# Kernel tuning notes

Measured on AMD Instinct MI355X. Metric: run time of the kernel, lower is better.

Reference implementation:

```python
import jax, jax.numpy as jnp
import numpy as np

NB_HEAD = 16
SIZE_PER_HEAD = 64


def setup_inputs() -> dict:
    key = jax.random.key(0)
    k1, k2 = jax.random.split(key)
    x = jax.random.normal(k1, (2, 2048, 1024), dtype=jnp.float32)
    kernel = jax.random.normal(k2, (3, 1024, NB_HEAD * SIZE_PER_HEAD), dtype=jnp.float32) * 0.02
    return {"x": x, "kernel": kernel}


def reference(x, kernel):
    B, S, D = x.shape
    H, dh = NB_HEAD, SIZE_PER_HEAD
    # QKV projections: [B,S,D] @ [D, H*dh] -> [B,S,H,dh] -> [B,H,S,dh]
    def proj(w):
        return jnp.einsum('bsd,de->bse', x, w).reshape(B, S, H, dh).transpose(0, 2, 1, 3)
    Q = proj(kernel[0])
    Ks = proj(kernel[1])
    V = proj(kernel[2])
    scores = jnp.einsum('bhqd,bhkd->bhqk', Q, Ks) / jnp.sqrt(jnp.float32(dh))
    attn = jax.nn.softmax(scores, axis=-1)
    z = jnp.einsum('bhqk,bhkd->bhqd', attn, V)  # [B,H,S,dh]
    return z.transpose(0, 2, 1, 3).reshape(B, S, H * dh)
```

## Files before the change

### kernel.cpp

```cpp
#include <hip/hip_runtime.h>
#include <hip/hip_bf16.h>

#define HB 16
#define DH 64
#define SQ 2048
#define BB 2

using f32x4 = __attribute__((ext_vector_type(4))) float;
using f32x16 = __attribute__((ext_vector_type(16))) float;
using s16x8 = __attribute__((ext_vector_type(8))) short;

__device__ __forceinline__ unsigned bfr(float f) {
    union { float f; unsigned u; } v; v.f = f;
    return (v.u + 0x7fffu + ((v.u >> 16) & 1u)) >> 16;
}
__device__ __forceinline__ unsigned pk2(float a, float b) { return bfr(a) | (bfr(b) << 16); }
__device__ __forceinline__ short f2bf(float f) { return (short)bfr(f); }

__device__ __forceinline__ int swz64(int r, int c) {
    return r * 64 + ((((c >> 3) ^ (r & 7)) & 7) << 3) + (c & 7);
}
__device__ __forceinline__ int swz32(int r, int c) {
    return r * 32 + ((((c >> 3) ^ ((r >> 1) & 3)) & 3) << 3) + (c & 7);
}

__device__ __forceinline__ void gll16(const short* g, short* l) {
    __builtin_amdgcn_global_load_lds(
        (const __attribute__((address_space(1))) unsigned int*)(uintptr_t)g,
        (__attribute__((address_space(3))) unsigned int*)(uintptr_t)l, 16, 0, 0);
}

__device__ __forceinline__ int swzT(int n, int k) {
    return n * 64 + ((((k >> 3) ^ ((n >> 2) & 7)) & 7) << 3) + (k & 7);
}
__global__ __launch_bounds__(256) void cvt_all(
    const float* __restrict__ x, const float* __restrict__ w,
    short* __restrict__ xb, short* __restrict__ wt)
{
    __shared__ short T[64 * 64];
    int bid = blockIdx.x;
    int t = threadIdx.x;
    if (bid < 2048) {
        int i = (bid * 256 + t) * 8;
        float4 v0 = *(const float4*)&x[i];
        float4 v1 = *(const float4*)&x[i + 4];
        uint4 u;
        u.x = pk2(v0.x, v0.y); u.y = pk2(v0.z, v0.w);
        u.z = pk2(v1.x, v1.y); u.w = pk2(v1.z, v1.w);
        *(uint4*)&xb[i] = u;
        return;
    }
    bid -= 2048;
    int nt = bid & 15, kt = (bid >> 4) & 15, p = bid >> 8;
    const float* wp = w + p * 1048576 + (kt * 64) * 1024 + nt * 64;
    short* wtp = wt + p * 1048576 + (nt * 64) * 1024 + kt * 64;
#pragma unroll
    for (int ps = 0; ps < 4; ps++) {
        int idx = ps * 1024 + t * 4;
        int r = idx >> 6, c = idx & 63;
        float4 v = *(const float4*)&wp[r * 1024 + c];
        T[swzT(c + 0, r)] = f2bf(v.x);
        T[swzT(c + 1, r)] = f2bf(v.y);
        T[swzT(c + 2, r)] = f2bf(v.z);
        T[swzT(c + 3, r)] = f2bf(v.w);
    }
    __syncthreads();
#pragma unroll
    for (int ps = 0; ps < 2; ps++) {
        int idx = ps * 2048 + t * 8;
        int n = idx >> 6, kc = idx & 63;
        s16x8 vv = *(const s16x8*)&T[swzT(n, kc)];
        *(s16x8*)&wtp[n * 1024 + kc] = vv;
    }
}

__global__ __launch_bounds__(512, 1) void qkv_gemm(
    const short* __restrict__ xb, const short* __restrict__ wt, short* __restrict__ ws)
{
    __shared__ short Xs[3][128 * 32];
    __shared__ short Ns[3][384 * 32];
    const int tid = threadIdx.x;
    const int wv = tid >> 6, ln = tid & 63;
    const int bid = blockIdx.x;
    const int swz = (bid & 7) * 32 + (bid >> 3);
    const int m0 = (swz & 31) * 128;
    const int n0 = (swz >> 5) * 128;

    const int wm = (wv >> 2) * 64, wn = (wv & 3) * 96;
    const int lr = ln & 15, lk = (ln >> 4) * 8;
    const int srow = tid >> 2;
    const int csw = (((tid & 3) ^ ((tid >> 3) & 3)) & 3) * 8;

    f32x4 acc[4][6] = {};

#define GSTAGE(k0_, bf_) do {                                                   \
        gll16(&xb[(m0 + srow) * 1024 + (k0_) + csw], &Xs[bf_][wv * 512]);       \
        _Pragma("unroll")                                                       \
        for (int p_ = 0; p_ < 3; p_++)                                          \
            gll16(&wt[p_ * 1048576 + (n0 + srow) * 1024 + (k0_) + csw],         \
                  &Ns[bf_][p_ * 4096 + wv * 512]);                              \
    } while (0)

#define GCOMP(bf_) do {                                                         \
        s16x8 af[4], bg[6];                                                     \
        _Pragma("unroll")                                                       \
        for (int i = 0; i < 4; i++)                                             \
            af[i] = *(const s16x8*)&Xs[bf_][swz32(wm + i * 16 + lr, lk)];       \
        _Pragma("unroll")                                                       \
        for (int j = 0; j < 6; j++)                                             \
            bg[j] = *(const s16x8*)&Ns[bf_][swz32(wn + j * 16 + lr, lk)];       \
        __builtin_amdgcn_s_setprio(1);                                          \
        _Pragma("unroll")                                                       \
        for (int i = 0; i < 4; i++)                                             \
            _Pragma("unroll")                                                   \
            for (int j = 0; j < 6; j++)                                         \
                acc[i][j] = __builtin_amdgcn_mfma_f32_16x16x32_bf16(af[i], bg[j], acc[i][j], 0, 0, 0); \
        __builtin_amdgcn_s_setprio(0);                                          \
    } while (0)

    GSTAGE(0, 0);
    GSTAGE(32, 1);
    int cur = 0;
    for (int t = 0; t < 31; t++) {
        asm volatile("s_waitcnt vmcnt(4)\n\ts_barrier" ::: "memory");
        int pre = cur + 2; if (pre >= 3) pre -= 3;
        if (t < 30) GSTAGE((t + 2) * 32, pre);
        GCOMP(cur);
        cur = (cur == 2) ? 0 : cur + 1;
    }
    asm volatile("s_waitcnt vmcnt(0)\n\ts_barrier" ::: "memory");
    GCOMP(cur);

    short* qws = ws;
    short* kws = ws + BB * HB * SQ * DH;
    short* vtw = ws + 2 * BB * HB * SQ * DH;
#pragma unroll
    for (int i = 0; i < 4; i++) {
#pragma unroll
        for (int r = 0; r < 4; r++) {
            int row = m0 + wm + i * 16 + (ln >> 4) * 4 + r;
            int b = row >> 11, s = row & 2047;
#pragma unroll
            for (int j = 0; j < 6; j++) {
                int c = wn + j * 16 + (ln & 15);
                int p = c >> 7;
                int gcol = n0 + (c & 127);
                int h = gcol >> 6, dhi = gcol & 63;
                float v = acc[i][j][r];
                if (p == 0)      qws[((b * HB + h) * SQ + s) * DH + dhi] = f2bf(v * 0.1803368801f);
                else if (p == 1) kws[((b * HB + h) * SQ + s) * DH + dhi] = f2bf(v);
                else             vtw[((b * HB + h) * DH + dhi) * SQ + s] = f2bf(v);
            }
        }
    }
#undef GSTAGE
#undef GCOMP
}

__global__ __launch_bounds__(512) void attn(
    const short* __restrict__ qws, const short* __restrict__ kws,
    const short* __restrict__ vtw, float* __restrict__ out)
{
    __shared__ __align__(16) short smem[32768];
    __shared__ float Lx[4][32];
    const int tid = threadIdx.x, wv = tid >> 6, ln = tid & 63;
    const int ws_ = wv & 3, g = wv >> 2;
    const int bid = blockIdx.x;
    const int swz = (bid & 7) * 64 + (bid >> 3);
    const int qt = swz & 15, bh = swz >> 4;
    const short* Q = qws + bh * SQ * DH;
    const short* K = kws + bh * SQ * DH;
    const short* VT = vtw + bh * DH * SQ;
    const int lq = ln & 31, lg = ln >> 5;
    const int q0w = qt * 128 + ws_ * 32;
    const int kvbase = g * 1024;

    const int klo = (ws_ * 8 + (ln >> 3)) * DH + (((ln & 7) ^ ((ln >> 3) & 7)) & 7) * 8;
    const int vr = ln >> 2;
    const int vlo = (ws_ * 16 + vr) * SQ + (((ln & 3) ^ ((vr >> 1) & 3)) & 3) * 8;

    s16x8 qf[4];
#pragma unroll
    for (int ks = 0; ks < 4; ks++)
        qf[ks] = *(const s16x8*)&Q[(q0w + lq) * DH + ks * 16 + lg * 8];

    f32x16 o0 = {}, o1 = {};
    float l = 0.f;

#define STAGE(t, bf_) do {                                          \
        short* Kd = smem + g * 16384 + (bf_) * 4096;                \
        const short* Kt = K + (kvbase + (t) * 32) * DH;             \
        const short* Vt = VT + kvbase + (t) * 32;                   \
        gll16(Kt + klo, Kd + ws_ * 512);                            \
        gll16(Vt + vlo, Kd + 2048 + ws_ * 512);                     \
    } while (0)

#define QKT(bf_, S_) do {                                                      \
        const short* Kr = smem + g * 16384 + (bf_) * 4096;                     \
        __builtin_amdgcn_s_setprio(1);                                         \
        _Pragma("unroll")                                                      \
        for (int ks = 0; ks < 4; ks++) {                                       \
            s16x8 ka = *(const s16x8*)&Kr[swz64(lq, ks * 16 + lg * 8)];        \
            S_ = __builtin_amdgcn_mfma_f32_32x32x16_bf16(ka, qf[ks], S_, 0, 0, 0); \
        }                                                                      \
        __builtin_amdgcn_s_setprio(0);                                         \
    } while (0)

#define SMPV(bf_, S_) do {                                                     \
        const short* Vr = smem + g * 16384 + (bf_) * 4096 + 2048;              \
        float p[16];                                                           \
        _Pragma("unroll")                                                      \
        for (int i = 0; i < 16; i++) p[i] = __builtin_amdgcn_exp2f(S_[i]);     \
        float a0 = 0.f, a1 = 0.f, a2 = 0.f, a3 = 0.f;                          \
        _Pragma("unroll")                                                      \
        for (int i = 0; i < 16; i += 4) {                                      \
            a0 += p[i]; a1 += p[i + 1]; a2 += p[i + 2]; a3 += p[i + 3];        \
        }                                                                      \
        l += (a0 + a1) + (a2 + a3);                                            \
        unsigned u[8];                                                         \
        _Pragma("unroll")                                                      \
        for (int qd = 0; qd < 4; qd++) {                                       \
            asm("v_cvt_pk_bf16_f32 %0, %1, %2" : "=v"(u[qd * 2]) : "v"(p[qd * 4 + 0]), "v"(p[qd * 4 + 1])); \
            asm("v_cvt_pk_bf16_f32 %0, %1, %2" : "=v"(u[qd * 2 + 1]) : "v"(p[qd * 4 + 2]), "v"(p[qd * 4 + 3])); \
        }                                                                      \
        _Pragma("unroll")                                                      \
        for (int m2 = 0; m2 < 2; m2++)                                         \
            _Pragma("unroll")                                                  \
            for (int j = 0; j < 2; j++)                                        \
                asm("v_permlane32_swap_b32 %0, %1"                             \
                    : "+v"(u[(2 * m2) * 2 + j]), "+v"(u[(2 * m2 + 1) * 2 + j])); \
        __builtin_amdgcn_s_setprio(1);                                         \
        _Pragma("unroll")                                                      \
        for (int ks = 0; ks < 2; ks++) {                                       \
            union { unsigned w[4]; s16x8 v; } pa;                              \
            pa.w[0] = u[4 * ks + 0];                                           \
            pa.w[1] = u[4 * ks + 1];                                           \
            pa.w[2] = u[4 * ks + 2];                                           \
            pa.w[3] = u[4 * ks + 3];                                           \
            s16x8 vb0 = *(const s16x8*)&Vr[swz32(lq, ks * 16 + lg * 8)];       \
            s16x8 vb1 = *(const s16x8*)&Vr[swz32(32 + lq, ks * 16 + lg * 8)];  \
            o0 = __builtin_amdgcn_mfma_f32_32x32x16_bf16(pa.v, vb0, o0, 0, 0, 0); \
            o1 = __builtin_amdgcn_mfma_f32_32x32x16_bf16(pa.v, vb1, o1, 0, 0, 0); \
        }                                                                      \
        __builtin_amdgcn_s_setprio(0);                                         \
    } while (0)

    STAGE(0, 0);
    STAGE(1, 1);
    STAGE(2, 2);
    asm volatile("s_waitcnt vmcnt(2)\n\ts_barrier" ::: "memory");
    f32x16 sA = {}, sB = {};
    QKT(0, sA);
#pragma unroll
    for (int t = 0; t < 32; t++) {
        if (t < 29) STAGE(t + 3, (t + 3) & 3);
        if (t < 31) {
            if (t & 1) QKT((t + 1) & 3, sA);
            else       QKT((t + 1) & 3, sB);
        }
        if (t & 1) SMPV(t & 3, sB);
        else       SMPV(t & 3, sA);
        if (t & 1) sB = (f32x16){};
        else       sA = (f32x16){};
        if (t < 29) asm volatile("s_waitcnt vmcnt(2)\n\ts_barrier" ::: "memory");
        else        asm volatile("s_waitcnt vmcnt(0)\n\ts_barrier" ::: "memory");
    }

    float lt = l + __shfl_xor(l, 32);
    float* Lf = (float*)smem;
    if (g == 1) {
#pragma unroll
        for (int r = 0; r < 16; r++) {
            Lf[ws_ * 1024 + r * 64 + ln] = o0[r];
            Lf[4096 + ws_ * 1024 + r * 64 + ln] = o1[r];
        }
        if (lg == 0) Lx[ws_][lq] = lt;
    }
    __syncthreads();
    if (g == 0) {
        float inv = 1.0f / (lt + Lx[ws_][lq]);
        const int b = bh >> 4, h = bh & 15;
#pragma unroll
        for (int r = 0; r < 16; r++) {
            int qrow = (r & 3) + 8 * (r >> 2) + 4 * lg;
            float iv = __shfl(inv, qrow);
            float* op = out + ((long)(b * SQ + q0w + qrow)) * 1024 + h * 64 + lq;
            op[0]  = (o0[r] + Lf[ws_ * 1024 + r * 64 + ln]) * iv;
            op[32] = (o1[r] + Lf[4096 + ws_ * 1024 + r * 64 + ln]) * iv;
        }
    }
#undef STAGE
#undef QKT
#undef SMPV
}

extern "C" void kernel_launch(void* const* d_in, const int* in_sizes, int n_in,
                              void* d_out, int out_size, void* d_ws, size_t ws_size,
                              hipStream_t stream) {
    const float* x = (const float*)d_in[0];
    const float* w = (const float*)d_in[1];
    short* ws = (short*)d_ws;
    short* xbf = (short*)d_out;
    short* wtb = (short*)d_out + 4194304;
    cvt_all<<<2816, 256, 0, stream>>>(x, w, xbf, wtb);
    qkv_gemm<<<256, 512, 0, stream>>>(xbf, wtb, ws);
    attn<<<512, 512, 0, stream>>>(ws, ws + BB * HB * SQ * DH,
                                  ws + 2 * BB * HB * SQ * DH, (float*)d_out);
}
```

Before: 89.99 us.

## Use K=64 double-buffered tiles in QKV GEMM instead of triple-buffered K=32

The QKV projection GEMM moves from a 3-stage pipeline with 32-wide K tiles to a 2-stage pipeline with 64-wide K tiles. Loads switch to a 64-column swizzle, and each barrier interval now covers two MFMA k-steps, halving the number of barriers. The trade-off is shallower prefetch, and the full __syncthreads with its implicit vmcnt(0) wait may expose global load latency.

```diff
diff --git a/kernel.cpp b/kernel.cpp
--- a/kernel.cpp
+++ b/kernel.cpp
@@ -77,8 +77,8 @@
 __global__ __launch_bounds__(512, 1) void qkv_gemm(
     const short* __restrict__ xb, const short* __restrict__ wt, short* __restrict__ ws)
 {
-    __shared__ short Xs[3][128 * 32];
-    __shared__ short Ns[3][384 * 32];
+    __shared__ short Xs[2][128 * 64];
+    __shared__ short Ns[2][384 * 64];
     const int tid = threadIdx.x;
     const int wv = tid >> 6, ln = tid & 63;
     const int bid = blockIdx.x;
@@ -88,48 +88,53 @@
 
     const int wm = (wv >> 2) * 64, wn = (wv & 3) * 96;
     const int lr = ln & 15, lk = (ln >> 4) * 8;
-    const int srow = tid >> 2;
-    const int csw = (((tid & 3) ^ ((tid >> 3) & 3)) & 3) * 8;
+    const int sr8 = ln >> 3;
+    const int csw = (((ln & 7) ^ ((ln >> 3) & 7)) & 7) * 8;
 
     f32x4 acc[4][6] = {};
 
 #define GSTAGE(k0_, bf_) do {                                                   \
-        gll16(&xb[(m0 + srow) * 1024 + (k0_) + csw], &Xs[bf_][wv * 512]);       \
         _Pragma("unroll")                                                       \
-        for (int p_ = 0; p_ < 3; p_++)                                          \
-            gll16(&wt[p_ * 1048576 + (n0 + srow) * 1024 + (k0_) + csw],         \
-                  &Ns[bf_][p_ * 4096 + wv * 512]);                              \
+        for (int c = 0; c < 2; c++)                                             \
+            gll16(&xb[(m0 + wv * 16 + c * 8 + sr8) * 1024 + (k0_) + csw],       \
+                  &Xs[bf_][(wv * 16 + c * 8) * 64]);                            \
+        _Pragma("unroll")                                                       \
+        for (int c = 0; c < 6; c++) {                                           \
+            int rb = wv * 48 + c * 8;                                           \
+            int p_ = rb >> 7, nr = rb & 127;                                    \
+            gll16(&wt[p_ * 1048576 + (n0 + nr + sr8) * 1024 + (k0_) + csw],     \
+                  &Ns[bf_][rb * 64]);                                           \
+        }                                                                       \
     } while (0)
 
 #define GCOMP(bf_) do {                                                         \
-        s16x8 af[4], bg[6];                                                     \
         _Pragma("unroll")                                                       \
-        for (int i = 0; i < 4; i++)                                             \
-            af[i] = *(const s16x8*)&Xs[bf_][swz32(wm + i * 16 + lr, lk)];       \
-        _Pragma("unroll")                                                       \
-        for (int j = 0; j < 6; j++)                                             \
-            bg[j] = *(const s16x8*)&Ns[bf_][swz32(wn + j * 16 + lr, lk)];       \
-        __builtin_amdgcn_s_setprio(1);                                          \
-        _Pragma("unroll")                                                       \
-        for (int i = 0; i < 4; i++)                                             \
+        for (int kk = 0; kk < 2; kk++) {                                        \
+            s16x8 af[4], bg[6];                                                 \
+            _Pragma("unroll")                                                   \
+            for (int i = 0; i < 4; i++)                                         \
+                af[i] = *(const s16x8*)&Xs[bf_][swz64(wm + i * 16 + lr, kk * 32 + lk)]; \
             _Pragma("unroll")                                                   \
             for (int j = 0; j < 6; j++)                                         \
-                acc[i][j] = __builtin_amdgcn_mfma_f32_16x16x32_bf16(af[i], bg[j], acc[i][j], 0, 0, 0); \
-        __builtin_amdgcn_s_setprio(0);                                          \
+                bg[j] = *(const s16x8*)&Ns[bf_][swz64(wn + j * 16 + lr, kk * 32 + lk)]; \
+            __builtin_amdgcn_s_setprio(1);                                      \
+            _Pragma("unroll")                                                   \
+            for (int i = 0; i < 4; i++)                                         \
+                _Pragma("unroll")                                               \
+                for (int j = 0; j < 6; j++)                                     \
+                    acc[i][j] = __builtin_amdgcn_mfma_f32_16x16x32_bf16(af[i], bg[j], acc[i][j], 0, 0, 0); \
+            __builtin_amdgcn_s_setprio(0);                                      \
+        }                                                                       \
     } while (0)
 
     GSTAGE(0, 0);
-    GSTAGE(32, 1);
-    int cur = 0;
-    for (int t = 0; t < 31; t++) {
-        asm volatile("s_waitcnt vmcnt(4)\n\ts_barrier" ::: "memory");
-        int pre = cur + 2; if (pre >= 3) pre -= 3;
-        if (t < 30) GSTAGE((t + 2) * 32, pre);
+    __syncthreads();
+    for (int t = 0; t < 16; t++) {
+        int cur = t & 1;
+        if (t < 15) GSTAGE((t + 1) * 64, cur ^ 1);
         GCOMP(cur);
-        cur = (cur == 2) ? 0 : cur + 1;
-    }
-    asm volatile("s_waitcnt vmcnt(0)\n\ts_barrier" ::: "memory");
-    GCOMP(cur);
+        __syncthreads();
+    }
 
     short* qws = ws;
     short* kws = ws + BB * HB * SQ * DH;
```

Result: no change. 88.81 us (-1.3%).
